# Kernel optimization log

Hardware: AMD Instinct MI355X
Metric: run time of the kernel (lower is better)

## Reference

```python
import jax, jax.numpy as jnp
import numpy as np

N, E = 50000, 800000
IN, HID, OUT = 128, 256, 40
EPS = 1e-5


def setup_inputs() -> dict:
    key = jax.random.key(0)
    ks = jax.random.split(key, 16)
    def glorot(k, shape):
        lim = float(np.sqrt(6.0 / (shape[0] + shape[1])))
        return jax.random.uniform(k, shape, jnp.float32, -lim, lim)
    return {
        "x": jax.random.normal(ks[0], (N, IN), jnp.float32),
        "edge_index": jax.random.randint(ks[1], (2, E), 0, N, jnp.int64),
        "W1": glorot(ks[2], (IN, HID)),  "b1": jnp.zeros((HID,), jnp.float32),
        "g1": jnp.ones((HID,), jnp.float32), "be1": jnp.zeros((HID,), jnp.float32),
        "W2": glorot(ks[3], (HID, HID)), "b2": jnp.zeros((HID,), jnp.float32),
        "g2": jnp.ones((HID,), jnp.float32), "be2": jnp.zeros((HID,), jnp.float32),
        "W3": glorot(ks[4], (HID, OUT)), "b3": jnp.zeros((OUT,), jnp.float32),
        "Wl": glorot(ks[5], (OUT, OUT)), "bl": jnp.zeros((OUT,), jnp.float32),
    }


def _gcn_conv(h, src, dst, norm, W, b, n):
    # PyG GCNConv: transform, then normalized scatter-add over edges (+self-loops)
    m = h @ W                                     # [N, d_out]
    msg = m[src] * norm[:, None]                  # gather + edge scale
    out = jax.ops.segment_sum(msg, dst, num_segments=n)
    return out + b


def _bn(h, g, b):
    # BatchNorm1d (training-mode batch stats, biased variance)
    mu = jnp.mean(h, axis=0)
    var = jnp.var(h, axis=0)
    return (h - mu) * jax.lax.rsqrt(var + EPS) * g + b


def reference(x, edge_index, W1, b1, g1, be1, W2, b2, g2, be2, W3, b3, Wl, bl):
    n = x.shape[0]
    loops = jnp.arange(n, dtype=edge_index.dtype)
    src = jnp.concatenate([edge_index[0], loops])
    dst = jnp.concatenate([edge_index[1], loops])
    deg = jax.ops.segment_sum(jnp.ones(src.shape[0], x.dtype), dst, num_segments=n)
    dinv = jnp.where(deg > 0, jax.lax.rsqrt(deg), 0.0)
    norm = dinv[src] * dinv[dst]

    h = jax.nn.relu(_bn(_gcn_conv(x, src, dst, norm, W1, b1, n), g1, be1))
    h = jax.nn.relu(_bn(_gcn_conv(h, src, dst, norm, W2, b2, n), g2, be2))
    h = _gcn_conv(h, src, dst, norm, W3, b3, n)
    h = h @ Wl + bl
    return jax.nn.log_softmax(h, axis=1)
```

## Files before the change

kernel.cpp:

```cpp
#include <hip/hip_runtime.h>
#include <hip/hip_bf16.h>
#include <math.h>

#define IN_DIM 128
#define HID 256
#define OUT_DIM 40
#define OUT_PAD 64
#define CAP 64
#define EPS 1e-5f

typedef __attribute__((ext_vector_type(8))) short short8;
typedef __attribute__((ext_vector_type(4))) float floatx4;

__device__ __forceinline__ float b2f(unsigned short u) {
    union { unsigned int i; float f; } c; c.i = ((unsigned int)u) << 16; return c.f;
}
__device__ __forceinline__ unsigned short f2b(float f) {
    union { float f; unsigned int i; } c; c.f = f;
    unsigned int r = c.i + 0x7FFF + ((c.i >> 16) & 1);
    return (unsigned short)(r >> 16);
}

union U8 { uint4 u; unsigned short s[8]; };


__global__ void fill1_k(const int* __restrict__ src, const int* __restrict__ dst,
                        int* __restrict__ cnt, int* __restrict__ col2, int E,
                        const float* __restrict__ W1, const float* __restrict__ W2,
                        const float* __restrict__ W3, const float* __restrict__ Wl,
                        const float* __restrict__ b3, const float* __restrict__ bl,
                        unsigned short* __restrict__ W1t, unsigned short* __restrict__ W2t,
                        unsigned short* __restrict__ W3lt, float* __restrict__ bias2,
                        float* __restrict__ stats1, float* __restrict__ stats2) {
    if (blockIdx.x < 1024) {
        for (int e = blockIdx.x * 256 + threadIdx.x; e < E; e += 1024 * 256) {
            int d = dst[e];
            int p = atomicAdd(&cnt[d], 1);
            if (p < CAP) col2[d * CAP + p] = src[e];
        }
    } else if (blockIdx.x < 1536) {
        const int n1 = 256 * 128, n2 = 256 * 256;
        int j = (blockIdx.x - 1024) * 256 + threadIdx.x;
        if (j < n1) {
            int n = j >> 7, k = j & 127;
            W1t[j] = f2b(W1[k * 256 + n]);
        } else if (j < n1 + n2) {
            int j2 = j - n1;
            int n = j2 >> 8, k = j2 & 255;
            W2t[j2] = f2b(W2[k * 256 + n]);
        } else {
            int j3 = j - n1 - n2;
            int n = j3 >> 8, k = j3 & 255;
            float acc = 0.f;
            if (n < OUT_DIM) {
                for (int q = 0; q < OUT_DIM; ++q)
                    acc += W3[k * OUT_DIM + q] * Wl[q * OUT_DIM + n];
            }
            W3lt[j3] = (n < OUT_DIM) ? f2b(acc) : 0;
            if (j3 < OUT_DIM) {
                float b = bl[j3];
                for (int q = 0; q < OUT_DIM; ++q) b += b3[q] * Wl[q * OUT_DIM + j3];
                bias2[j3] = b;
            }
        }
    } else {
        int t = threadIdx.x;
        stats1[t] = 0.f; stats1[256 + t] = 0.f;
        stats2[t] = 0.f; stats2[256 + t] = 0.f;
    }
}


__global__ void conv_k(const float* __restrict__ x, const int* __restrict__ cnt,
                       float* __restrict__ dinv, unsigned short* __restrict__ xb, int N) {
    size_t nx = (size_t)N * 32;
    for (size_t i = blockIdx.x * 256 + threadIdx.x; i < nx; i += (size_t)1024 * 256) {
        size_t row = i >> 5;
        float dv = rsqrtf((float)(cnt[row] + 1));
        if ((i & 31) == 0) dinv[row] = dv;
        float4 v = ((const float4*)x)[i];
        ushort4 o;
        o.x = f2b(v.x * dv); o.y = f2b(v.y * dv);
        o.z = f2b(v.z * dv); o.w = f2b(v.w * dv);
        ((ushort4*)xb)[i] = o;
    }
}


template <bool BN, bool STATS>
__global__ __launch_bounds__(256) void gemm_bf16(const unsigned short* __restrict__ A,
                                                 const unsigned short* __restrict__ Bt,
                                                 unsigned short* __restrict__ C,
                                                 const float* __restrict__ rowscale,
                                                 const float* __restrict__ bias,
                                                 const float* __restrict__ bnstats,
                                                 const float* __restrict__ g,
                                                 const float* __restrict__ be,
                                                 float* __restrict__ gstats,
                                                 float invN,
                                                 int M, int Nc, int K, int ldc) {
    __shared__ unsigned short As[128][40];
    __shared__ unsigned short Bs[128][40];
    __shared__ float s_sc[HID], s_sh[HID];
    __shared__ float ls1[128], ls2[128];
    int tid = threadIdx.x;
    if (BN) {
        float mu = bnstats[tid] * invN;
        float var = bnstats[HID + tid] * invN - mu * mu;
        float sc = g[tid] * rsqrtf(var + EPS);
        s_sc[tid] = sc;
        s_sh[tid] = be[tid] - mu * sc;
    }
    if (STATS && tid < 128) { ls1[tid] = 0.f; ls2[tid] = 0.f; }
    __syncthreads();

    int wave = tid >> 6, lane = tid & 63;
    int wm = wave >> 1, wn = wave & 1;
    int quad = lane >> 4, r16 = lane & 15;
    int row0 = blockIdx.y * 128, col0 = blockIdx.x * 128;

    floatx4 acc[4][4] = {};

    for (int k0 = 0; k0 < K; k0 += 32) {
#pragma unroll
        for (int i = 0; i < 2; ++i) {
            int idx = tid * 2 + i;
            int r = idx >> 2;
            int ko = (idx & 3) * 8;
            int ar = min(row0 + r, M - 1);
            U8 ra;
            ra.u = *(const uint4*)&A[(size_t)ar * K + k0 + ko];
            if (BN) {
#pragma unroll
                for (int j = 0; j < 8; ++j) {
                    int kk = k0 + ko + j;
                    float v = b2f(ra.s[j]) * s_sc[kk] + s_sh[kk];
                    ra.s[j] = f2b(fmaxf(v, 0.f));
                }
            }
            *(uint4*)&As[r][ko] = ra.u;
            *(uint4*)&Bs[r][ko] = *(const uint4*)&Bt[(size_t)(col0 + r) * K + k0 + ko];
        }
        __syncthreads();
        short8 a[4], b[4];
#pragma unroll
        for (int mt = 0; mt < 4; ++mt)
            a[mt] = *(const short8*)&As[wm * 64 + mt * 16 + r16][quad * 8];
#pragma unroll
        for (int nt = 0; nt < 4; ++nt)
            b[nt] = *(const short8*)&Bs[wn * 64 + nt * 16 + r16][quad * 8];
#pragma unroll
        for (int mt = 0; mt < 4; ++mt)
#pragma unroll
            for (int nt = 0; nt < 4; ++nt)
                acc[mt][nt] = __builtin_amdgcn_mfma_f32_16x16x32_bf16(a[mt], b[nt], acc[mt][nt], 0, 0, 0);
        __syncthreads();
    }

    float s1[4] = {0.f, 0.f, 0.f, 0.f}, s2[4] = {0.f, 0.f, 0.f, 0.f};
#pragma unroll
    for (int mt = 0; mt < 4; ++mt) {
#pragma unroll
        for (int r = 0; r < 4; ++r) {
            int row = row0 + wm * 64 + mt * 16 + quad * 4 + r;
            if (row >= M) continue;
            float dv = rowscale ? rowscale[row] : 1.f;
#pragma unroll
            for (int nt = 0; nt < 4; ++nt) {
                int colg = col0 + wn * 64 + nt * 16 + r16;
                if (colg < Nc) {
                    float v = acc[mt][nt][r] * dv + (bias ? bias[colg] : 0.f);
                    C[(size_t)row * ldc + colg] = f2b(v);
                    if (STATS) { s1[nt] += v; s2[nt] += v * v; }
                }
            }
        }
    }
    if (STATS) {
#pragma unroll
        for (int nt = 0; nt < 4; ++nt) {
            s1[nt] += __shfl_xor(s1[nt], 16); s1[nt] += __shfl_xor(s1[nt], 32);
            s2[nt] += __shfl_xor(s2[nt], 16); s2[nt] += __shfl_xor(s2[nt], 32);
            if (quad == 0) {
                int cj = wn * 64 + nt * 16 + r16;
                atomicAdd(&ls1[cj], s1[nt]);
                atomicAdd(&ls2[cj], s2[nt]);
            }
        }
        __syncthreads();
        if (tid < 128) {
            int cg = col0 + tid;
            atomicAdd(&gstats[cg], ls1[tid]);
            atomicAdd(&gstats[HID + cg], ls2[tid]);
        }
    }
}


__global__ __launch_bounds__(256, 8) void agg_h(const unsigned short* __restrict__ m,
                                                const int* __restrict__ col2,
                                                const int* __restrict__ cnt,
                                                const float* __restrict__ dinv,
                                                const float* __restrict__ bias,
                                                unsigned short* __restrict__ out,
                                                int N) {
    int v = blockIdx.x * 4 + (threadIdx.x >> 6);
    if (v >= N) return;
    int lane = threadIdx.x & 63;
    int half = lane >> 5;
    int c0 = (lane & 31) * 8;
    float dv = dinv[v];
    const int* col = col2 + v * CAP;
    int end = min(cnt[v], CAP);
    float a[8] = {};
    if (half == 0) {
        U8 r; r.u = *(const uint4*)&m[(size_t)v * HID + c0];
#pragma unroll
        for (int k = 0; k < 8; ++k) a[k] = b2f(r.s[k]);
    }
    int e = 0;
    for (; e + 8 <= end; e += 8) {
        int idx[4];
#pragma unroll
        for (int j = 0; j < 4; ++j) idx[j] = col[e + 2 * j + half];
        U8 rr[4];
#pragma unroll
        for (int j = 0; j < 4; ++j)
            rr[j].u = *(const uint4*)&m[(size_t)idx[j] * HID + c0];
#pragma unroll
        for (int j = 0; j < 4; ++j)
#pragma unroll
            for (int k = 0; k < 8; ++k) a[k] += b2f(rr[j].s[k]);
    }
    for (; e < end; e += 2) {
        int t = e + half;
        if (t < end) {
            U8 r; r.u = *(const uint4*)&m[(size_t)col[t] * HID + c0];
#pragma unroll
            for (int k = 0; k < 8; ++k) a[k] += b2f(r.s[k]);
        }
    }
#pragma unroll
    for (int k = 0; k < 8; ++k) a[k] += __shfl_xor(a[k], 32);
    if (half == 0) {
        U8 o;
#pragma unroll
        for (int k = 0; k < 8; ++k) o.s[k] = f2b(a[k] * dv + bias[c0 + k]);
        *(uint4*)&out[(size_t)v * HID + c0] = o.u;
    }
}

__global__ __launch_bounds__(256, 8) void agg_x(const unsigned short* __restrict__ m,
                                                const int* __restrict__ col2,
                                                const int* __restrict__ cnt,
                                                const float* __restrict__ dinv,
                                                unsigned short* __restrict__ out,
                                                int N) {
    int v = blockIdx.x * 4 + (threadIdx.x >> 6);
    if (v >= N) return;
    int lane = threadIdx.x & 63;
    int q = lane >> 4;
    int c0 = (lane & 15) * 8;
    float dv = dinv[v];
    const int* col = col2 + v * CAP;
    int end = min(cnt[v], CAP);
    float a[8] = {};
    if (q == 0) {
        U8 r; r.u = *(const uint4*)&m[(size_t)v * IN_DIM + c0];
#pragma unroll
        for (int k = 0; k < 8; ++k) a[k] = b2f(r.s[k]);
    }
    int e = 0;
    for (; e + 8 <= end; e += 8) {
        int idx[2];
#pragma unroll
        for (int j = 0; j < 2; ++j) idx[j] = col[e + 4 * j + q];
        U8 rr[2];
#pragma unroll
        for (int j = 0; j < 2; ++j)
            rr[j].u = *(const uint4*)&m[(size_t)idx[j] * IN_DIM + c0];
#pragma unroll
        for (int j = 0; j < 2; ++j)
#pragma unroll
            for (int k = 0; k < 8; ++k) a[k] += b2f(rr[j].s[k]);
    }
    for (; e < end; e += 4) {
        int t = e + q;
        if (t < end) {
            U8 r; r.u = *(const uint4*)&m[(size_t)col[t] * IN_DIM + c0];
#pragma unroll
            for (int k = 0; k < 8; ++k) a[k] += b2f(r.s[k]);
        }
    }
#pragma unroll
    for (int k = 0; k < 8; ++k) {
        a[k] += __shfl_xor(a[k], 16);
        a[k] += __shfl_xor(a[k], 32);
    }
    if (q == 0) {
        U8 o;
#pragma unroll
        for (int k = 0; k < 8; ++k) o.s[k] = f2b(a[k] * dv);
        *(uint4*)&out[(size_t)v * IN_DIM + c0] = o.u;
    }
}

__global__ __launch_bounds__(256, 8) void agg_o_ls(const unsigned short* __restrict__ m,
                                                   const int* __restrict__ col2,
                                                   const int* __restrict__ cnt,
                                                   const float* __restrict__ dinv,
                                                   const float* __restrict__ bias2,
                                                   float* __restrict__ out,
                                                   int N) {
    int v = blockIdx.x * 4 + (threadIdx.x >> 6);
    if (v >= N) return;
    int lane = threadIdx.x & 63;
    int slot = lane >> 3;
    int li = lane & 7;
    int c0 = li * 8;
    float dv = dinv[v];
    const int* col = col2 + v * CAP;
    int end = min(cnt[v], CAP);
    float a[8] = {};
    if (slot == 0) {
        U8 r; r.u = *(const uint4*)&m[(size_t)v * OUT_PAD + c0];
#pragma unroll
        for (int k = 0; k < 8; ++k) a[k] = b2f(r.s[k]);
    }
    int e = 0;
    for (; e + 16 <= end; e += 16) {
        int idx[2];
        idx[0] = col[e + slot];
        idx[1] = col[e + 8 + slot];
        U8 rr[2];
#pragma unroll
        for (int j = 0; j < 2; ++j)
            rr[j].u = *(const uint4*)&m[(size_t)idx[j] * OUT_PAD + c0];
#pragma unroll
        for (int j = 0; j < 2; ++j)
#pragma unroll
            for (int k = 0; k < 8; ++k) a[k] += b2f(rr[j].s[k]);
    }
    for (; e < end; e += 8) {
        int t = e + slot;
        if (t < end) {
            U8 r; r.u = *(const uint4*)&m[(size_t)col[t] * OUT_PAD + c0];
#pragma unroll
            for (int k = 0; k < 8; ++k) a[k] += b2f(r.s[k]);
        }
    }
#pragma unroll
    for (int k = 0; k < 8; ++k) {
        a[k] += __shfl_xor(a[k], 8);
        a[k] += __shfl_xor(a[k], 16);
        a[k] += __shfl_xor(a[k], 32);
    }
    bool valid = (li < 5);
    float mx = -INFINITY;
#pragma unroll
    for (int k = 0; k < 8; ++k) {
        float val = valid ? (a[k] * dv + bias2[c0 + k]) : -INFINITY;
        a[k] = val;
        mx = fmaxf(mx, val);
    }
    mx = fmaxf(mx, __shfl_xor(mx, 1));
    mx = fmaxf(mx, __shfl_xor(mx, 2));
    mx = fmaxf(mx, __shfl_xor(mx, 4));
    float s = 0.f;
    if (valid) {
#pragma unroll
        for (int k = 0; k < 8; ++k) s += expf(a[k] - mx);
    }
    s += __shfl_xor(s, 1);
    s += __shfl_xor(s, 2);
    s += __shfl_xor(s, 4);
    float ls = mx + logf(s);
    if (slot == 0 && valid) {
        float4 o0, o1;
        o0.x = a[0] - ls; o0.y = a[1] - ls; o0.z = a[2] - ls; o0.w = a[3] - ls;
        o1.x = a[4] - ls; o1.y = a[5] - ls; o1.z = a[6] - ls; o1.w = a[7] - ls;
        float* p = &out[(size_t)v * OUT_DIM + c0];
        *(float4*)p = o0;
        *(float4*)(p + 4) = o1;
    }
}


__global__ __launch_bounds__(256) void bn_stats(const unsigned short* __restrict__ h,
                                                float* __restrict__ stats, int N) {
    __shared__ float ls[8][2][256];
    int t = threadIdx.x;
    int walker = t >> 5;
    int c0 = (t & 31) * 8;
    int r0 = blockIdx.x * 128;
    int rend = min(r0 + 128, N);
    float s1[8] = {}, s2[8] = {};
    for (int r = r0 + walker; r < rend; r += 8) {
        U8 x; x.u = *(const uint4*)&h[(size_t)r * HID + c0];
#pragma unroll
        for (int k = 0; k < 8; ++k) {
            float v = b2f(x.s[k]);
            s1[k] += v; s2[k] += v * v;
        }
    }
#pragma unroll
    for (int k = 0; k < 8; ++k) {
        ls[walker][0][c0 + k] = s1[k];
        ls[walker][1][c0 + k] = s2[k];
    }
    __syncthreads();
    float a1 = 0.f, a2 = 0.f;
#pragma unroll
    for (int w = 0; w < 8; ++w) { a1 += ls[w][0][t]; a2 += ls[w][1][t]; }
    atomicAdd(&stats[t], a1);
    atomicAdd(&stats[HID + t], a2);
}


extern "C" void kernel_launch(void* const* d_in, const int* in_sizes, int n_in,
                              void* d_out, int out_size, void* d_ws, size_t ws_size,
                              hipStream_t stream) {
    const float* x   = (const float*)d_in[0];
    const int*  eidx = (const int*)d_in[1];
    const float* W1 = (const float*)d_in[2];
    const float* b1 = (const float*)d_in[3];
    const float* g1 = (const float*)d_in[4];
    const float* be1 = (const float*)d_in[5];
    const float* W2 = (const float*)d_in[6];
    const float* b2 = (const float*)d_in[7];
    const float* g2 = (const float*)d_in[8];
    const float* be2 = (const float*)d_in[9];
    const float* W3 = (const float*)d_in[10];
    const float* b3 = (const float*)d_in[11];
    const float* Wl = (const float*)d_in[12];
    const float* bl = (const float*)d_in[13];
    float* out = (float*)d_out;

    const int N = in_sizes[0] / IN_DIM;
    const int E = in_sizes[1] / 2;
    const int* src = eidx;
    const int* dst = eidx + E;

    size_t off = 0;
    char* ws = (char*)d_ws;
    auto carve = [&](size_t bytes) -> void* {
        void* p = ws + off;
        off += (bytes + 255) & ~(size_t)255;
        return p;
    };
    int*   cnt  = (int*)carve((size_t)N * 4);
    float* stats1 = (float*)carve((size_t)2 * HID * 4);
    float* stats2 = (float*)carve((size_t)2 * HID * 4);
    float* dinv = (float*)carve((size_t)N * 4);
    int*   col2 = (int*)carve((size_t)N * CAP * 4);
    unsigned short* xb   = (unsigned short*)carve((size_t)N * IN_DIM * 2);
    unsigned short* axb  = (unsigned short*)carve((size_t)N * IN_DIM * 2);
    unsigned short* W1t  = (unsigned short*)carve((size_t)256 * IN_DIM * 2);
    unsigned short* W2t  = (unsigned short*)carve((size_t)256 * HID * 2);
    unsigned short* W3lt = (unsigned short*)carve((size_t)128 * HID * 2);
    float* bias2 = (float*)carve((size_t)OUT_DIM * 4);
    unsigned short* mbuf = (unsigned short*)carve((size_t)N * HID * 2);
    unsigned short* hbuf = (unsigned short*)carve((size_t)N * HID * 2);

    hipMemsetAsync(cnt, 0, (size_t)N * 4, stream);
    fill1_k<<<1537, 256, 0, stream>>>(src, dst, cnt, col2, E,
                                      W1, W2, W3, Wl, b3, bl,
                                      W1t, W2t, W3lt, bias2, stats1, stats2);
    conv_k<<<1024, 256, 0, stream>>>(x, cnt, dinv, xb, N);

    int mblocks = (N + 127) / 128;
    dim3 gg1(2, mblocks), gg3(1, mblocks);
    int nodeBlocks = (N + 3) / 4;
    float invN = 1.f / (float)N;

    agg_x<<<nodeBlocks, 256, 0, stream>>>(xb, col2, cnt, dinv, axb, N);
    gemm_bf16<false, true><<<gg1, 256, 0, stream>>>(axb, W1t, hbuf, nullptr, b1,
                                                    nullptr, nullptr, nullptr, stats1,
                                                    invN, N, HID, IN_DIM, HID);

    gemm_bf16<true, false><<<gg1, 256, 0, stream>>>(hbuf, W2t, mbuf, dinv, nullptr,
                                                    stats1, g1, be1, nullptr,
                                                    invN, N, HID, HID, HID);
    agg_h<<<nodeBlocks, 256, 0, stream>>>(mbuf, col2, cnt, dinv, b2, hbuf, N);
    bn_stats<<<(N + 127) / 128, 256, 0, stream>>>(hbuf, stats2, N);

    gemm_bf16<true, false><<<gg3, 256, 0, stream>>>(hbuf, W3lt, mbuf, dinv, nullptr,
                                                    stats2, g2, be2, nullptr,
                                                    invN, N, OUT_PAD, HID, OUT_PAD);
    agg_o_ls<<<nodeBlocks, 256, 0, stream>>>(mbuf, col2, cnt, dinv, bias2, out, N);
}
```

Baseline: 405.8 us.

## Replace LDS-tiled GEMM with single-wave direct-load MFMA kernel and separate BN stats

The block-level GEMM that staged A and B tiles through shared memory is replaced with a one-wave-per-block kernel computing a 64x64 tile. Each lane loads its MFMA fragments directly from global memory, removing LDS staging and barriers. Layer-1 batch statistics are no longer fused into the GEMM epilogue and are computed by a separate bn_stats launch instead. The trade-off is more global/L2 traffic from lost cross-wave reuse, plus an extra kernel and a re-read of the hidden buffer.

```diff
diff --git a/kernel.cpp b/kernel.cpp
--- a/kernel.cpp
+++ b/kernel.cpp
@@ -22,6 +22,7 @@
 }
 
 union U8 { uint4 u; unsigned short s[8]; };
+union F8 { short8 v; unsigned short s[8]; uint4 u; };
 
 
 __global__ void fill1_k(const int* __restrict__ src, const int* __restrict__ dst,
@@ -87,111 +88,84 @@
 }
 
 
-template <bool BN, bool STATS>
-__global__ __launch_bounds__(256) void gemm_bf16(const unsigned short* __restrict__ A,
-                                                 const unsigned short* __restrict__ Bt,
-                                                 unsigned short* __restrict__ C,
-                                                 const float* __restrict__ rowscale,
-                                                 const float* __restrict__ bias,
-                                                 const float* __restrict__ bnstats,
-                                                 const float* __restrict__ g,
-                                                 const float* __restrict__ be,
-                                                 float* __restrict__ gstats,
-                                                 float invN,
-                                                 int M, int Nc, int K, int ldc) {
-    __shared__ unsigned short As[128][40];
-    __shared__ unsigned short Bs[128][40];
+template <bool BN>
+__global__ __launch_bounds__(64, 3) void gemm_w(const unsigned short* __restrict__ A,
+                                                const unsigned short* __restrict__ Bt,
+                                                unsigned short* __restrict__ C,
+                                                const float* __restrict__ rowscale,
+                                                const float* __restrict__ bias,
+                                                const float* __restrict__ bnstats,
+                                                const float* __restrict__ g,
+                                                const float* __restrict__ be,
+                                                float invN,
+                                                int M, int Nc, int K, int ldc) {
     __shared__ float s_sc[HID], s_sh[HID];
-    __shared__ float ls1[128], ls2[128];
-    int tid = threadIdx.x;
+    int lane = threadIdx.x;
     if (BN) {
-        float mu = bnstats[tid] * invN;
-        float var = bnstats[HID + tid] * invN - mu * mu;
-        float sc = g[tid] * rsqrtf(var + EPS);
-        s_sc[tid] = sc;
-        s_sh[tid] = be[tid] - mu * sc;
-    }
-    if (STATS && tid < 128) { ls1[tid] = 0.f; ls2[tid] = 0.f; }
-    __syncthreads();
-
-    int wave = tid >> 6, lane = tid & 63;
-    int wm = wave >> 1, wn = wave & 1;
-    int quad = lane >> 4, r16 = lane & 15;
-    int row0 = blockIdx.y * 128, col0 = blockIdx.x * 128;
+        for (int t = lane; t < K; t += 64) {
+            float mu = bnstats[t] * invN;
+            float var = bnstats[HID + t] * invN - mu * mu;
+            float sc = g[t] * rsqrtf(var + EPS);
+            s_sc[t] = sc;
+            s_sh[t] = be[t] - mu * sc;
+        }
+        __syncthreads();
+    }
+    int r16 = lane & 15, quad = lane >> 4;
+    int row0 = blockIdx.y * 64, col0 = blockIdx.x * 64;
+
+    int arow[4];
+#pragma unroll
+    for (int mt = 0; mt < 4; ++mt) arow[mt] = min(row0 + mt * 16 + r16, M - 1);
 
     floatx4 acc[4][4] = {};
 
     for (int k0 = 0; k0 < K; k0 += 32) {
-#pragma unroll
-        for (int i = 0; i < 2; ++i) {
-            int idx = tid * 2 + i;
-            int r = idx >> 2;
-            int ko = (idx & 3) * 8;
-            int ar = min(row0 + r, M - 1);
-            U8 ra;
-            ra.u = *(const uint4*)&A[(size_t)ar * K + k0 + ko];
-            if (BN) {
+        int ka = k0 + quad * 8;
+        F8 a[4], b[4];
+#pragma unroll
+        for (int mt = 0; mt < 4; ++mt)
+            a[mt].u = *(const uint4*)&A[(size_t)arow[mt] * K + ka];
+#pragma unroll
+        for (int nt = 0; nt < 4; ++nt)
+            b[nt].u = *(const uint4*)&Bt[(size_t)(col0 + nt * 16 + r16) * K + ka];
+        if (BN) {
+            float4 sc0 = *(const float4*)&s_sc[ka];
+            float4 sc1 = *(const float4*)&s_sc[ka + 4];
+            float4 sh0 = *(const float4*)&s_sh[ka];
+            float4 sh1 = *(const float4*)&s_sh[ka + 4];
+            float sc[8] = {sc0.x, sc0.y, sc0.z, sc0.w, sc1.x, sc1.y, sc1.z, sc1.w};
+            float sh[8] = {sh0.x, sh0.y, sh0.z, sh0.w, sh1.x, sh1.y, sh1.z, sh1.w};
+#pragma unroll
+            for (int mt = 0; mt < 4; ++mt)
 #pragma unroll
                 for (int j = 0; j < 8; ++j) {
-                    int kk = k0 + ko + j;
-                    float v = b2f(ra.s[j]) * s_sc[kk] + s_sh[kk];
-                    ra.s[j] = f2b(fmaxf(v, 0.f));
+                    float f = b2f(a[mt].s[j]) * sc[j] + sh[j];
+                    a[mt].s[j] = f2b(fmaxf(f, 0.f));
                 }
-            }
-            *(uint4*)&As[r][ko] = ra.u;
-            *(uint4*)&Bs[r][ko] = *(const uint4*)&Bt[(size_t)(col0 + r) * K + k0 + ko];
-        }
-        __syncthreads();
-        short8 a[4], b[4];
+        }
 #pragma unroll
         for (int mt = 0; mt < 4; ++mt)
-            a[mt] = *(const short8*)&As[wm * 64 + mt * 16 + r16][quad * 8];
-#pragma unroll
-        for (int nt = 0; nt < 4; ++nt)
-            b[nt] = *(const short8*)&Bs[wn * 64 + nt * 16 + r16][quad * 8];
-#pragma unroll
-        for (int mt = 0; mt < 4; ++mt)
 #pragma unroll
             for (int nt = 0; nt < 4; ++nt)
-                acc[mt][nt] = __builtin_amdgcn_mfma_f32_16x16x32_bf16(a[mt], b[nt], acc[mt][nt], 0, 0, 0);
-        __syncthreads();
-    }
-
-    float s1[4] = {0.f, 0.f, 0.f, 0.f}, s2[4] = {0.f, 0.f, 0.f, 0.f};
+                acc[mt][nt] = __builtin_amdgcn_mfma_f32_16x16x32_bf16(a[mt].v, b[nt].v, acc[mt][nt], 0, 0, 0);
+    }
+
 #pragma unroll
     for (int mt = 0; mt < 4; ++mt) {
 #pragma unroll
         for (int r = 0; r < 4; ++r) {
-            int row = row0 + wm * 64 + mt * 16 + quad * 4 + r;
+            int row = row0 + mt * 16 + quad * 4 + r;
             if (row >= M) continue;
             float dv = rowscale ? rowscale[row] : 1.f;
 #pragma unroll
             for (int nt = 0; nt < 4; ++nt) {
-                int colg = col0 + wn * 64 + nt * 16 + r16;
+                int colg = col0 + nt * 16 + r16;
                 if (colg < Nc) {
                     float v = acc[mt][nt][r] * dv + (bias ? bias[colg] : 0.f);
                     C[(size_t)row * ldc + colg] = f2b(v);
-                    if (STATS) { s1[nt] += v; s2[nt] += v * v; }
                 }
             }
-        }
-    }
-    if (STATS) {
-#pragma unroll
-        for (int nt = 0; nt < 4; ++nt) {
-            s1[nt] += __shfl_xor(s1[nt], 16); s1[nt] += __shfl_xor(s1[nt], 32);
-            s2[nt] += __shfl_xor(s2[nt], 16); s2[nt] += __shfl_xor(s2[nt], 32);
-            if (quad == 0) {
-                int cj = wn * 64 + nt * 16 + r16;
-                atomicAdd(&ls1[cj], s1[nt]);
-                atomicAdd(&ls2[cj], s2[nt]);
-            }
-        }
-        __syncthreads();
-        if (tid < 128) {
-            int cg = col0 + tid;
-            atomicAdd(&gstats[cg], ls1[tid]);
-            atomicAdd(&gstats[HID + cg], ls2[tid]);
         }
     }
 }
@@ -468,24 +442,24 @@
                                       W1t, W2t, W3lt, bias2, stats1, stats2);
     conv_k<<<1024, 256, 0, stream>>>(x, cnt, dinv, xb, N);
 
-    int mblocks = (N + 127) / 128;
-    dim3 gg1(2, mblocks), gg3(1, mblocks);
+    int mb64 = (N + 63) / 64;
     int nodeBlocks = (N + 3) / 4;
     float invN = 1.f / (float)N;
 
     agg_x<<<nodeBlocks, 256, 0, stream>>>(xb, col2, cnt, dinv, axb, N);
-    gemm_bf16<false, true><<<gg1, 256, 0, stream>>>(axb, W1t, hbuf, nullptr, b1,
-                                                    nullptr, nullptr, nullptr, stats1,
+    gemm_w<false><<<dim3(4, mb64), 64, 0, stream>>>(axb, W1t, hbuf, nullptr, b1,
+                                                    nullptr, nullptr, nullptr,
                                                     invN, N, HID, IN_DIM, HID);
-
-    gemm_bf16<true, false><<<gg1, 256, 0, stream>>>(hbuf, W2t, mbuf, dinv, nullptr,
-                                                    stats1, g1, be1, nullptr,
-                                                    invN, N, HID, HID, HID);
+    bn_stats<<<(N + 127) / 128, 256, 0, stream>>>(hbuf, stats1, N);
+
+    gemm_w<true><<<dim3(4, mb64), 64, 0, stream>>>(hbuf, W2t, mbuf, dinv, nullptr,
+                                                   stats1, g1, be1,
+                                                   invN, N, HID, HID, HID);
     agg_h<<<nodeBlocks, 256, 0, stream>>>(mbuf, col2, cnt, dinv, b2, hbuf, N);
     bn_stats<<<(N + 127) / 128, 256, 0, stream>>>(hbuf, stats2, N);
 
-    gemm_bf16<true, false><<<gg3, 256, 0, stream>>>(hbuf, W3lt, mbuf, dinv, nullptr,
-                                                    stats2, g2, be2, nullptr,
-                                                    invN, N, OUT_PAD, HID, OUT_PAD);
+    gemm_w<true><<<dim3(1, mb64), 64, 0, stream>>>(hbuf, W3lt, mbuf, dinv, nullptr,
+                                                   stats2, g2, be2,
+                                                   invN, N, OUT_PAD, HID, OUT_PAD);
     agg_o_ls<<<nodeBlocks, 256, 0, stream>>>(mbuf, col2, cnt, dinv, bias2, out, N);
 }
```

Measured after the change: 414.6 us. 2.2% more time.
